# Kernel optimization log

Measured on AMD Instinct MI355X. Metric: run time of the kernel, lower is better.

Reference implementation:

```python
import jax, jax.numpy as jnp
import numpy as np

B, S, E = 4, 4096, 128  # batch, seq_len, embedding_dim (quaternion groups)
D = 4 * E               # flattened feature dim fed to the Linear layers


def setup_inputs() -> dict:
    key = jax.random.key(0)
    ks = jax.random.split(key, 9)
    scale_w = 1.0 / np.sqrt(D).astype(np.float32)
    return {
        "query": jax.random.normal(ks[0], (B, S, E, 4), dtype=jnp.float32),
        "key": jax.random.normal(ks[1], (B, S, E, 4), dtype=jnp.float32),
        "value": jax.random.normal(ks[2], (B, S, E, 4), dtype=jnp.float32),
        "Wq": jax.random.normal(ks[3], (D, D), dtype=jnp.float32) * scale_w,
        "bq": jax.random.normal(ks[4], (D,), dtype=jnp.float32) * 0.01,
        "Wk": jax.random.normal(ks[5], (D, D), dtype=jnp.float32) * scale_w,
        "bk": jax.random.normal(ks[6], (D,), dtype=jnp.float32) * 0.01,
        "Wv": jax.random.normal(ks[7], (D, D), dtype=jnp.float32) * scale_w,
        "bv": jax.random.normal(ks[8], (D,), dtype=jnp.float32) * 0.01,
    }


def reference(query, key, value, Wq, bq, Wk, bk, Wv, bv):
    b, s = query.shape[0], query.shape[1]
    e = query.shape[2]  # embedding_dim
    # flatten quaternion dim: [B,S,E,4] -> [B,S,4E]
    q = query.reshape(b, s, -1)
    k = key.reshape(b, key.shape[1], -1)
    v = value.reshape(b, value.shape[1], -1)
    # torch nn.Linear: x @ W^T + bias
    Q = (q @ Wq.T + bq).reshape(b, s, -1, 4)
    K = (k @ Wk.T + bk).reshape(b, key.shape[1], -1, 4)
    V = (v @ Wv.T + bv).reshape(b, value.shape[1], -1, 4)
    # full QK^T over quaternion-grouped dims: [B,S,S]
    scores = jnp.einsum('bseq,bkeq->bsk', Q, K) / jnp.sqrt(jnp.float32(e))
    weights = jax.nn.softmax(scores, axis=-1)
    # faithful to the source: weights are summed over k and scale V at position s
    output = jnp.einsum('bsk,bseq->bseq', weights, V)
    return output, weights
```

## Files before the change

### kernel.cpp

```cpp
#include <hip/hip_runtime.h>
#include <cstdint>

typedef _Float16 h1;
typedef _Float16 h4 __attribute__((ext_vector_type(4)));
typedef _Float16 h8 __attribute__((ext_vector_type(8)));
typedef float    f4 __attribute__((ext_vector_type(4)));
typedef float    f32x4 __attribute__((ext_vector_type(4)));

#define NB 4
#define SL 4096
#define DD 512
#define MM (NB*SL)
#define SHIFT 12.0f

__global__ __launch_bounds__(256) void convert_all(
    const float* __restrict__ Xq, const float* __restrict__ Xk, const float* __restrict__ Xv,
    const float* __restrict__ Wq, const float* __restrict__ Wk, const float* __restrict__ Wv,
    h1* __restrict__ Xh, h1* __restrict__ Wh)
{
    const int xper = MM*DD/4;
    const int wper = DD*DD/4;
    const int xtot = 3*xper;
    int i = blockIdx.x * 256 + threadIdx.x;
    const float* src;
    h1* dst;
    int j;
    if (i < xtot) {
        int mat = i / xper; j = i - mat*xper;
        src = (mat==0) ? Xq : (mat==1 ? Xk : Xv);
        dst = Xh + (size_t)mat*MM*DD;
    } else {
        int t = i - xtot;
        if (t >= 3*wper) return;
        int mat = t / wper; j = t - mat*wper;
        src = (mat==0) ? Wq : (mat==1 ? Wk : Wv);
        dst = Wh + (size_t)mat*DD*DD;
    }
    f4 v = ((const f4*)src)[j];
    h4 hv;
    hv[0]=(h1)v[0]; hv[1]=(h1)v[1]; hv[2]=(h1)v[2]; hv[3]=(h1)v[3];
    ((h4*)dst)[j] = hv;
}

__device__ __forceinline__ void stage_tile(const h1* __restrict__ gbase,
                                           h1* lds, int w, int l)
{
    #pragma unroll
    for (int j = 0; j < 4; j++) {
        const int cc  = w*4 + j;
        const int row = cc*8 + (l >> 3);
        const int sc  = (l & 7) ^ (l >> 3);
        const h1* src = gbase + (size_t)row * DD + sc*8;
        void* dst = (char*)lds + cc*1024;
        __builtin_amdgcn_global_load_lds(
            (const __attribute__((address_space(1))) uint32_t*)src,
            (__attribute__((address_space(3))) uint32_t*)dst, 16, 0, 0);
    }
}

__device__ __forceinline__ h8 lds_frag(const h1* lds, int row, int lc)
{
    const int chunk = lc ^ (row & 7);
    return *(const h8*)(lds + row*64 + chunk*8);
}

__global__ __launch_bounds__(256) void proj_gemm(
    const h1* __restrict__ Xh, const h1* __restrict__ Wh,
    const float* __restrict__ bq, const float* __restrict__ bk, const float* __restrict__ bv,
    h1* __restrict__ Qh, h1* __restrict__ Kh, float* __restrict__ Vout)
{
    const int prj = blockIdx.z;
    const h1* __restrict__ X    = Xh + (size_t)prj * MM * DD;
    const h1* __restrict__ W    = Wh + (size_t)prj * DD * DD;
    const float* __restrict__ bias = (prj==0) ? bq : (prj==1 ? bk : bv);

    const int m0 = blockIdx.y * 128;
    const int n0 = blockIdx.x * 128;

    __shared__ h1 As[128*64];
    __shared__ h1 Bs[128*64];

    const int tid  = threadIdx.x;
    const int lane = tid & 63;
    const int wid  = tid >> 6;
    const int wm = wid >> 1, wn = wid & 1;
    const int g  = lane >> 4, c = lane & 15;

    f32x4 acc[4][4];
    #pragma unroll
    for (int i = 0; i < 4; i++)
        #pragma unroll
        for (int j = 0; j < 4; j++) acc[i][j] = (f32x4){0.f, 0.f, 0.f, 0.f};

    for (int k0 = 0; k0 < DD; k0 += 64) {
        __syncthreads();
        stage_tile(X + (size_t)m0 * DD + k0, As, wid, lane);
        stage_tile(W + (size_t)n0 * DD + k0, Bs, wid, lane);
        __syncthreads();
        #pragma unroll
        for (int kk = 0; kk < 2; kk++) {
            h8 af[4], bf[4];
            #pragma unroll
            for (int mf = 0; mf < 4; mf++) af[mf] = lds_frag(As, wm*64 + mf*16 + c, kk*4 + g);
            #pragma unroll
            for (int nf = 0; nf < 4; nf++) bf[nf] = lds_frag(Bs, wn*64 + nf*16 + c, kk*4 + g);
            #pragma unroll
            for (int mf = 0; mf < 4; mf++)
                #pragma unroll
                for (int nf = 0; nf < 4; nf++)
                    acc[mf][nf] = __builtin_amdgcn_mfma_f32_16x16x32_f16(af[mf], bf[nf], acc[mf][nf], 0, 0, 0);
        }
    }

    float bv4[4];
    #pragma unroll
    for (int nf = 0; nf < 4; nf++) bv4[nf] = bias[n0 + wn*64 + nf*16 + c];

    #pragma unroll
    for (int mf = 0; mf < 4; mf++) {
        #pragma unroll
        for (int i = 0; i < 4; i++) {
            const int row = m0 + wm*64 + mf*16 + g*4 + i;
            #pragma unroll
            for (int nf = 0; nf < 4; nf++) {
                const int col = n0 + wn*64 + nf*16 + c;
                float vv = acc[mf][nf][i] + bv4[nf];
                if (prj == 0)      Qh[(size_t)row*DD + col] = (h1)vv;
                else if (prj == 1) Kh[(size_t)row*DD + col] = (h1)vv;
                else               Vout[(size_t)row*DD + col] = vv;
            }
        }
    }
}

__global__ __launch_bounds__(256) void scores_gemm(
    const h1* __restrict__ Qh, const h1* __restrict__ Kh,
    h1* __restrict__ Eh,
    float* __restrict__ partial)
{
    const int b  = blockIdx.z;
    const int m0 = blockIdx.y * 128;
    const int n0 = blockIdx.x * 128;
    const h1* __restrict__ Qb = Qh + (size_t)b * SL * DD;
    const h1* __restrict__ Kb = Kh + (size_t)b * SL * DD;

    __shared__ h1 As[128*64];
    __shared__ h1 Bs[128*64];

    const int tid  = threadIdx.x;
    const int lane = tid & 63;
    const int wid  = tid >> 6;
    const int wm = wid >> 1, wn = wid & 1;
    const int g  = lane >> 4, c = lane & 15;

    f32x4 acc[4][4];
    #pragma unroll
    for (int i = 0; i < 4; i++)
        #pragma unroll
        for (int j = 0; j < 4; j++) acc[i][j] = (f32x4){0.f, 0.f, 0.f, 0.f};

    for (int k0 = 0; k0 < DD; k0 += 64) {
        __syncthreads();
        stage_tile(Qb + (size_t)m0 * DD + k0, As, wid, lane);
        stage_tile(Kb + (size_t)n0 * DD + k0, Bs, wid, lane);
        __syncthreads();
        #pragma unroll
        for (int kk = 0; kk < 2; kk++) {
            h8 af[4], bf[4];
            #pragma unroll
            for (int mf = 0; mf < 4; mf++) af[mf] = lds_frag(As, wm*64 + mf*16 + c, kk*4 + g);
            #pragma unroll
            for (int nf = 0; nf < 4; nf++) bf[nf] = lds_frag(Bs, wn*64 + nf*16 + c, kk*4 + g);
            #pragma unroll
            for (int mf = 0; mf < 4; mf++)
                #pragma unroll
                for (int nf = 0; nf < 4; nf++)
                    acc[mf][nf] = __builtin_amdgcn_mfma_f32_16x16x32_f16(af[mf], bf[nf], acc[mf][nf], 0, 0, 0);
        }
    }

    const float inv_scale = 0.08838834764831845f;
    #pragma unroll
    for (int mf = 0; mf < 4; mf++) {
        #pragma unroll
        for (int i = 0; i < 4; i++) {
            const int row = m0 + wm*64 + mf*16 + g*4 + i;
            h1* erow = Eh + ((size_t)b * SL + row) * SL;
            float rsum = 0.f;
            #pragma unroll
            for (int nf = 0; nf < 4; nf++) {
                const int col = n0 + wn*64 + nf*16 + c;
                float e = __expf(fmaf(acc[mf][nf][i], inv_scale, -SHIFT));
                erow[col] = (h1)e;
                rsum += e;
            }
            #pragma unroll
            for (int off = 1; off < 16; off <<= 1) rsum += __shfl_xor(rsum, off);
            if (c == 0)
                partial[((size_t)b * SL + row) * 64 + blockIdx.x * 2 + wn] = rsum;
        }
    }
}

__global__ __launch_bounds__(256) void rowsum_inv(
    const float* __restrict__ partial, float* __restrict__ invrow)
{
    int row = blockIdx.x * 256 + threadIdx.x;
    const f4* p = (const f4*)(partial + (size_t)row * 64);
    float s = 0.f;
    #pragma unroll
    for (int i = 0; i < 16; i++) { f4 v = p[i]; s += v[0] + v[1] + v[2] + v[3]; }
    invrow[row] = 1.0f / s;
}

__global__ __launch_bounds__(256) void normalize_k(
    const h1* __restrict__ Eh, const float* __restrict__ invrow,
    float* __restrict__ Wout)
{
    const size_t total8 = (size_t)NB * SL * SL / 8;
    size_t i = (size_t)blockIdx.x * blockDim.x + threadIdx.x;
    const size_t stride = (size_t)gridDim.x * blockDim.x;
    for (; i < total8; i += stride) {
        const int row = (int)(i >> 9);
        h8 v = ((const h8*)Eh)[i];
        const float s = invrow[row];
        f4 o0, o1;
        #pragma unroll
        for (int j = 0; j < 4; j++) { o0[j] = (float)v[j] * s; o1[j] = (float)v[4+j] * s; }
        ((f4*)Wout)[i*2]   = o0;
        ((f4*)Wout)[i*2+1] = o1;
    }
}

extern "C" void kernel_launch(void* const* d_in, const int* in_sizes, int n_in,
                              void* d_out, int out_size, void* d_ws, size_t ws_size,
                              hipStream_t stream)
{
    const float* q  = (const float*)d_in[0];
    const float* k  = (const float*)d_in[1];
    const float* v  = (const float*)d_in[2];
    const float* Wq = (const float*)d_in[3];
    const float* bq = (const float*)d_in[4];
    const float* Wk = (const float*)d_in[5];
    const float* bk = (const float*)d_in[6];
    const float* Wv = (const float*)d_in[7];
    const float* bv = (const float*)d_in[8];

    float* out  = (float*)d_out;
    float* Vout = out;
    float* Wout = out + (size_t)MM * DD;

    char* ws = (char*)d_ws;
    h1* Xh = (h1*)ws;
    h1* Wh = (h1*)(ws + (size_t)3*MM*DD*2);
    h1* Qh = (h1*)((char*)Wh + (size_t)3*DD*DD*2);
    h1* Kh = (h1*)((char*)Qh + (size_t)MM*DD*2);
    float* partial = (float*)((char*)Kh + (size_t)MM*DD*2);
    float* invrow  = (float*)((char*)partial + (size_t)MM*64*4);
    h1* Eh = (h1*)((char*)invrow + (size_t)MM*4);

    const int conv_chunks = (3*MM*DD + 3*DD*DD) / 4;
    convert_all<<<(conv_chunks + 255)/256, 256, 0, stream>>>(q, k, v, Wq, Wk, Wv, Xh, Wh);
    proj_gemm<<<dim3(4, 128, 3), 256, 0, stream>>>(Xh, Wh, bq, bk, bv, Qh, Kh, Vout);
    scores_gemm<<<dim3(32, 32, NB), 256, 0, stream>>>(Qh, Kh, Eh, partial);
    rowsum_inv<<<MM / 256, 256, 0, stream>>>(partial, invrow);
    normalize_k<<<2048, 256, 0, stream>>>(Eh, invrow, Wout);
}
```

Measured before the change: 296.7 us.

## Rewrite scores GEMM as 256x256 double-buffered 8-wave pipelined kernel

Replaces the 128x128 single-buffered scores GEMM with a 256x256 tile kernel using 512 threads, double-buffered LDS, prefetch of the next K-tile during MFMA phases, setprio around MFMA bursts, and XCD-aware block swizzling. It aims to hide global load latency and raise data reuse per block. In exchange it uses more LDS (128KB) and more registers (a larger accumulator per wave), which reduces occupancy, and there are now many more barriers per K-step. The layout of the partial row sums stays compatible with the 64 slots per row.

New measurement: 286.5 us. 3.5% less time.

```diff
diff --git a/kernel.cpp b/kernel.cpp
--- a/kernel.cpp
+++ b/kernel.cpp
@@ -58,6 +58,21 @@
     }
 }
 
+__device__ __forceinline__ void stage_half(const h1* __restrict__ gbase,
+                                           char* ldsbase, int w, int l)
+{
+    #pragma unroll
+    for (int j = 0; j < 2; j++) {
+        const int cc  = w*2 + j;
+        const int row = cc*8 + (l >> 3);
+        const int sc  = (l & 7) ^ (l >> 3);
+        const h1* src = gbase + (size_t)row * DD + sc*8;
+        __builtin_amdgcn_global_load_lds(
+            (const __attribute__((address_space(1))) uint32_t*)src,
+            (__attribute__((address_space(3))) uint32_t*)(ldsbase + cc*1024), 16, 0, 0);
+    }
+}
+
 __device__ __forceinline__ h8 lds_frag(const h1* lds, int row, int lc)
 {
     const int chunk = lc ^ (row & 7);
@@ -133,58 +148,101 @@
     }
 }
 
-__global__ __launch_bounds__(256) void scores_gemm(
+__global__ __launch_bounds__(512) void scores_gemm_8ph(
     const h1* __restrict__ Qh, const h1* __restrict__ Kh,
     h1* __restrict__ Eh,
     float* __restrict__ partial)
 {
-    const int b  = blockIdx.z;
-    const int m0 = blockIdx.y * 128;
-    const int n0 = blockIdx.x * 128;
+    const int orig = blockIdx.x;
+    const int swz  = (orig & 7) * 128 + (orig >> 3);
+    const int b  = swz >> 8;
+    const int t_ = swz & 255;
+    const int ty = t_ >> 4;
+    const int tx = t_ & 15;
+    const int m0 = ty * 256;
+    const int n0 = tx * 256;
     const h1* __restrict__ Qb = Qh + (size_t)b * SL * DD;
     const h1* __restrict__ Kb = Kh + (size_t)b * SL * DD;
 
-    __shared__ h1 As[128*64];
-    __shared__ h1 Bs[128*64];
+    __shared__ h1 Albuf[2*256*64];
+    __shared__ h1 Blbuf[2*256*64];
+    const int SLOT_H = 256*64;
+    const int SLOT_B = SLOT_H*2;
 
     const int tid  = threadIdx.x;
     const int lane = tid & 63;
     const int wid  = tid >> 6;
-    const int wm = wid >> 1, wn = wid & 1;
+    const int wm = wid >> 2;
+    const int wn = wid & 3;
     const int g  = lane >> 4, c = lane & 15;
 
-    f32x4 acc[4][4];
-    #pragma unroll
-    for (int i = 0; i < 4; i++)
+    f32x4 acc[8][4];
+    #pragma unroll
+    for (int i = 0; i < 8; i++)
         #pragma unroll
         for (int j = 0; j < 4; j++) acc[i][j] = (f32x4){0.f, 0.f, 0.f, 0.f};
 
-    for (int k0 = 0; k0 < DD; k0 += 64) {
-        __syncthreads();
-        stage_tile(Qb + (size_t)m0 * DD + k0, As, wid, lane);
-        stage_tile(Kb + (size_t)n0 * DD + k0, Bs, wid, lane);
-        __syncthreads();
-        #pragma unroll
-        for (int kk = 0; kk < 2; kk++) {
-            h8 af[4], bf[4];
-            #pragma unroll
-            for (int mf = 0; mf < 4; mf++) af[mf] = lds_frag(As, wm*64 + mf*16 + c, kk*4 + g);
-            #pragma unroll
-            for (int nf = 0; nf < 4; nf++) bf[nf] = lds_frag(Bs, wn*64 + nf*16 + c, kk*4 + g);
-            #pragma unroll
-            for (int mf = 0; mf < 4; mf++)
+    stage_half(Qb + (size_t)m0*DD,            (char*)Albuf,          wid, lane);
+    stage_half(Qb + (size_t)(m0+128)*DD,      (char*)Albuf + 16384,  wid, lane);
+    stage_half(Kb + (size_t)n0*DD,            (char*)Blbuf,          wid, lane);
+    stage_half(Kb + (size_t)(n0+128)*DD,      (char*)Blbuf + 16384,  wid, lane);
+    asm volatile("s_waitcnt vmcnt(0)" ::: "memory");
+    __builtin_amdgcn_s_barrier();
+
+    for (int kt = 0; kt < 8; ++kt) {
+        const int cur = kt & 1;
+        const h1* Abase = Albuf + cur*SLOT_H;
+        const h1* Bbase = Blbuf + cur*SLOT_H;
+        #pragma unroll
+        for (int q = 0; q < 4; q++) {
+            const int mh = q >> 1, nh = q & 1;
+
+            h8 af[4][2], bf[2][2];
+            #pragma unroll
+            for (int fm = 0; fm < 4; fm++)
                 #pragma unroll
-                for (int nf = 0; nf < 4; nf++)
-                    acc[mf][nf] = __builtin_amdgcn_mfma_f32_16x16x32_f16(af[mf], bf[nf], acc[mf][nf], 0, 0, 0);
+                for (int ks = 0; ks < 2; ks++)
+                    af[fm][ks] = lds_frag(Abase, wm*128 + (mh*4+fm)*16 + c, ks*4 + g);
+            #pragma unroll
+            for (int fn = 0; fn < 2; fn++)
+                #pragma unroll
+                for (int ks = 0; ks < 2; ks++)
+                    bf[fn][ks] = lds_frag(Bbase, wn*64 + (nh*2+fn)*16 + c, ks*4 + g);
+
+            if (q == 0 && kt < 7) {
+                const int k0n = (kt+1) * 64;
+                char* Adst = (char*)Albuf + (cur^1)*SLOT_B;
+                char* Bdst = (char*)Blbuf + (cur^1)*SLOT_B;
+                stage_half(Qb + (size_t)m0*DD + k0n,       Adst,         wid, lane);
+                stage_half(Qb + (size_t)(m0+128)*DD + k0n, Adst + 16384, wid, lane);
+                stage_half(Kb + (size_t)n0*DD + k0n,       Bdst,         wid, lane);
+                stage_half(Kb + (size_t)(n0+128)*DD + k0n, Bdst + 16384, wid, lane);
+            }
+
+            __builtin_amdgcn_s_barrier();
+            asm volatile("s_waitcnt lgkmcnt(0)" ::: "memory");
+            __builtin_amdgcn_sched_barrier(0);
+            __builtin_amdgcn_s_setprio(1);
+            #pragma unroll
+            for (int fm = 0; fm < 4; fm++)
+                #pragma unroll
+                for (int fn = 0; fn < 2; fn++)
+                    #pragma unroll
+                    for (int ks = 0; ks < 2; ks++)
+                        acc[mh*4+fm][nh*2+fn] = __builtin_amdgcn_mfma_f32_16x16x32_f16(
+                            af[fm][ks], bf[fn][ks], acc[mh*4+fm][nh*2+fn], 0, 0, 0);
+            __builtin_amdgcn_s_setprio(0);
+            if (q == 3) asm volatile("s_waitcnt vmcnt(0)" ::: "memory");
+            __builtin_amdgcn_s_barrier();
         }
     }
 
     const float inv_scale = 0.08838834764831845f;
     #pragma unroll
-    for (int mf = 0; mf < 4; mf++) {
+    for (int mf = 0; mf < 8; mf++) {
         #pragma unroll
         for (int i = 0; i < 4; i++) {
-            const int row = m0 + wm*64 + mf*16 + g*4 + i;
+            const int row = m0 + wm*128 + mf*16 + g*4 + i;
             h1* erow = Eh + ((size_t)b * SL + row) * SL;
             float rsum = 0.f;
             #pragma unroll
@@ -197,7 +255,7 @@
             #pragma unroll
             for (int off = 1; off < 16; off <<= 1) rsum += __shfl_xor(rsum, off);
             if (c == 0)
-                partial[((size_t)b * SL + row) * 64 + blockIdx.x * 2 + wn] = rsum;
+                partial[((size_t)b * SL + row) * 64 + tx * 4 + wn] = rsum;
         }
     }
 }
@@ -262,7 +320,7 @@
     const int conv_chunks = (3*MM*DD + 3*DD*DD) / 4;
     convert_all<<<(conv_chunks + 255)/256, 256, 0, stream>>>(q, k, v, Wq, Wk, Wv, Xh, Wh);
     proj_gemm<<<dim3(4, 128, 3), 256, 0, stream>>>(Xh, Wh, bq, bk, bv, Qh, Kh, Vout);
-    scores_gemm<<<dim3(32, 32, NB), 256, 0, stream>>>(Qh, Kh, Eh, partial);
+    scores_gemm_8ph<<<1024, 512, 0, stream>>>(Qh, Kh, Eh, partial);
     rowsum_inv<<<MM / 256, 256, 0, stream>>>(partial, invrow);
     normalize_k<<<2048, 256, 0, stream>>>(Eh, invrow, Wout);
 }
```
